# Kernel optimization log

Hardware: AMD Instinct MI355X
Metric: run time of the kernel (lower is better)

The kernel has to match this reference:

```python
import jax, jax.numpy as jnp
import numpy as np
from jax import lax

BN_EPS = 1e-3  # keras BatchNormalization default
DN = ('NHWC', 'HWIO', 'NHWC')


def setup_inputs() -> dict:
    key = jax.random.key(0)
    ks = jax.random.split(key, 8)
    B, H, W, C = 16, 224, 224, 96
    K = 3
    x = jax.random.normal(ks[0], (B, H, W, C), dtype=jnp.float32)
    dw_kernel = jax.random.normal(ks[1], (K, K, 1, C), dtype=jnp.float32) * 0.1
    dw_bias = jnp.zeros((C,), dtype=jnp.float32)
    pw_kernel = jax.random.normal(ks[2], (1, 1, C, C), dtype=jnp.float32) * 0.1
    pw_bias = jnp.zeros((C,), dtype=jnp.float32)
    gamma = jax.random.uniform(ks[3], (C,), dtype=jnp.float32, minval=0.5, maxval=1.5)
    beta = jax.random.normal(ks[4], (C,), dtype=jnp.float32) * 0.1
    moving_mean = jax.random.normal(ks[5], (C,), dtype=jnp.float32) * 0.1
    moving_var = jax.random.uniform(ks[6], (C,), dtype=jnp.float32, minval=0.5, maxval=1.5)
    return {
        'x': x, 'dw_kernel': dw_kernel, 'dw_bias': dw_bias,
        'pw_kernel': pw_kernel, 'pw_bias': pw_bias,
        'gamma': gamma, 'beta': beta,
        'moving_mean': moving_mean, 'moving_var': moving_var,
    }


def reference(x, dw_kernel, dw_bias, pw_kernel, pw_bias, gamma, beta, moving_mean, moving_var):
    C = x.shape[-1]
    stride = 1
    # ReLU at the start of the op
    y = jax.nn.relu(x)
    # Depthwise conv: feature_group_count = C, kernel HWIO = (K, K, 1, C)
    y = lax.conv_general_dilated(
        y, dw_kernel, window_strides=(stride, stride), padding='SAME',
        dimension_numbers=DN, feature_group_count=C)
    y = y + dw_bias
    # Pointwise 1x1 conv to C_curr channels
    y = lax.conv_general_dilated(
        y, pw_kernel, window_strides=(1, 1), padding='SAME',
        dimension_numbers=DN)
    y = y + pw_bias
    # BatchNormalization (inference mode: use moving statistics)
    inv = gamma * lax.rsqrt(moving_var + BN_EPS)
    y = y * inv + (beta - moving_mean * inv)
    return y
```

## Files before the change

kernel.cpp:

```cpp
#include <hip/hip_runtime.h>
#include <hip/hip_bf16.h>


#define BATCH 16
#define HH 224
#define WWD 224
#define CC 96
#define NPIX (BATCH*HH*WWD)
#define TILE 64
#define NBLK (NPIX/TILE)
#define NTHREADS 384
#define PAD 104

typedef __attribute__((ext_vector_type(8))) short short8;
typedef __attribute__((ext_vector_type(4))) float f32x4;

__device__ __forceinline__ unsigned short f2bf(float f){
    union{float f; unsigned u;} v; v.f = f;
    unsigned r = v.u + 0x7fffu + ((v.u >> 16) & 1u);
    return (unsigned short)(r >> 16);
}

__global__ __launch_bounds__(NTHREADS) void sepconv_kernel(
    const float* __restrict__ x,
    const float* __restrict__ dwk,
    const float* __restrict__ dwb,
    const float* __restrict__ pwk,
    const float* __restrict__ pwb,
    const float* __restrict__ gma,
    const float* __restrict__ bta,
    const float* __restrict__ mmean,
    const float* __restrict__ mvar,
    float* __restrict__ out)
{
    __shared__ __align__(16) unsigned short s_dw[TILE][PAD];
    __shared__ __align__(16) unsigned short s_pwT[CC][PAD];
    __shared__ float s_scale[CC];
    __shared__ float s_shift[CC];

    const int t  = threadIdx.x;
    const int p0 = blockIdx.x * TILE;

    for (int e = t; e < CC*CC; e += NTHREADS) {
        int ci = e / CC;
        int co = e - ci*CC;
        s_pwT[co][ci] = f2bf(pwk[e]);
    }
    if (t < CC) {
        float g  = gma[t];
        float be = bta[t];
        float mu = mmean[t];
        float va = mvar[t];
        float pb = pwb[t];
        float sc = g / sqrtf(va + 1e-3f);
        s_scale[t] = sc;
        s_shift[t] = (pb - mu) * sc + be;
    }

    #pragma unroll
    for (int it = 0; it < 2; ++it) {
        int i  = t + it*NTHREADS;
        int px = i / 12;
        int cg = i - px*12;
        int c0 = cg*8;
        int p  = p0 + px;
        int b  = p / (HH*WWD);
        int rem = p - b*(HH*WWD);
        int h  = rem / WWD;
        int w  = rem - h*WWD;

        float acc[8];
        {
            float4 b0 = *reinterpret_cast<const float4*>(dwb + c0);
            float4 b1 = *reinterpret_cast<const float4*>(dwb + c0 + 4);
            acc[0]=b0.x; acc[1]=b0.y; acc[2]=b0.z; acc[3]=b0.w;
            acc[4]=b1.x; acc[5]=b1.y; acc[6]=b1.z; acc[7]=b1.w;
        }
        #pragma unroll
        for (int kh = -1; kh <= 1; ++kh) {
            int h2 = h + kh;
            if ((unsigned)h2 >= HH) continue;
            #pragma unroll
            for (int kw = -1; kw <= 1; ++kw) {
                int w2 = w + kw;
                if ((unsigned)w2 >= WWD) continue;
                const float* xp = x + (size_t)((b*HH + h2)*WWD + w2)*CC + c0;
                const float* wp = dwk + ((kh+1)*3 + (kw+1))*CC + c0;
                float4 x0 = *reinterpret_cast<const float4*>(xp);
                float4 x1 = *reinterpret_cast<const float4*>(xp + 4);
                float4 w0 = *reinterpret_cast<const float4*>(wp);
                float4 w1 = *reinterpret_cast<const float4*>(wp + 4);
                acc[0] += fmaxf(x0.x, 0.f) * w0.x;
                acc[1] += fmaxf(x0.y, 0.f) * w0.y;
                acc[2] += fmaxf(x0.z, 0.f) * w0.z;
                acc[3] += fmaxf(x0.w, 0.f) * w0.w;
                acc[4] += fmaxf(x1.x, 0.f) * w1.x;
                acc[5] += fmaxf(x1.y, 0.f) * w1.y;
                acc[6] += fmaxf(x1.z, 0.f) * w1.z;
                acc[7] += fmaxf(x1.w, 0.f) * w1.w;
            }
        }
        uint4 sv;
        sv.x = (unsigned)f2bf(acc[0]) | ((unsigned)f2bf(acc[1]) << 16);
        sv.y = (unsigned)f2bf(acc[2]) | ((unsigned)f2bf(acc[3]) << 16);
        sv.z = (unsigned)f2bf(acc[4]) | ((unsigned)f2bf(acc[5]) << 16);
        sv.w = (unsigned)f2bf(acc[6]) | ((unsigned)f2bf(acc[7]) << 16);
        *reinterpret_cast<uint4*>(&s_dw[px][c0]) = sv;
    }

    __syncthreads();

    const int wave = t >> 6;
    const int lane = t & 63;
    const int col  = lane & 15;
    const int quad = lane >> 4;
    const int co   = wave*16 + col;

    short8 bfr[3];
    #pragma unroll
    for (int ks = 0; ks < 3; ++ks)
        bfr[ks] = *reinterpret_cast<const short8*>(&s_pwT[co][ks*32 + quad*8]);

    const float sc = s_scale[co];
    const float sh = s_shift[co];

    #pragma unroll
    for (int mt = 0; mt < 4; ++mt) {
        f32x4 acc = {0.f, 0.f, 0.f, 0.f};
        #pragma unroll
        for (int ks = 0; ks < 3; ++ks) {
            short8 afr = *reinterpret_cast<const short8*>(&s_dw[mt*16 + col][ks*32 + quad*8]);
            acc = __builtin_amdgcn_mfma_f32_16x16x32_bf16(afr, bfr[ks], acc, 0, 0, 0);
        }
        int prow = p0 + mt*16 + quad*4;
        #pragma unroll
        for (int r = 0; r < 4; ++r) {
            float v = acc[r]*sc + sh;
            out[(size_t)(prow + r)*CC + co] = v;
        }
    }
}

extern "C" void kernel_launch(void* const* d_in, const int* in_sizes, int n_in,
                              void* d_out, int out_size, void* d_ws, size_t ws_size,
                              hipStream_t stream)
{
    sepconv_kernel<<<NBLK, NTHREADS, 0, stream>>>(
        (const float*)d_in[0],
        (const float*)d_in[1],
        (const float*)d_in[2],
        (const float*)d_in[3],
        (const float*)d_in[4],
        (const float*)d_in[5],
        (const float*)d_in[6],
        (const float*)d_in[7],
        (const float*)d_in[8],
        (float*)d_out);
}
```

Measured before the change: 688.9 us.

## Use persistent XCD-banded waves computing depthwise conv directly into MFMA fragments

Replaces the one-block-per-64-pixel launch with a persistent grid of 1024 blocks. Each wave processes 16-pixel row tiles, and tiles are assigned in contiguous bands per XCD so neighbouring rows share L2. The depthwise result is computed straight into registers already in MFMA A-fragment layout, which removes the shared-memory staging buffer and its barrier. The pointwise weights are staged and converted once per block instead of once per 64 pixels. In exchange, each lane issues more scattered loads, register pressure is higher, and the band mapping assumes a particular XCD scheduling order.

Result: slower. 755.6 us (+9.7%).

```diff
diff --git a/kernel.cpp b/kernel.cpp
--- a/kernel.cpp
+++ b/kernel.cpp
@@ -6,10 +6,15 @@
 #define HH 224
 #define WWD 224
 #define CC 96
-#define NPIX (BATCH*HH*WWD)
-#define TILE 64
-#define NBLK (NPIX/TILE)
-#define NTHREADS 384
+#define ROWS (BATCH*HH)
+#define TPR 14
+#define NTILES (ROWS*TPR)
+#define NTHREADS 256
+#define WAVES 4
+#define NBLOCKS 1024
+#define NXCD 8
+#define TILES_PER_BAND (NTILES/NXCD)
+#define WAVES_PER_BAND ((NBLOCKS/NXCD)*WAVES)
 #define PAD 104
 
 typedef __attribute__((ext_vector_type(8))) short short8;
@@ -21,7 +26,28 @@
     return (unsigned short)(r >> 16);
 }
 
-__global__ __launch_bounds__(NTHREADS) void sepconv_kernel(
+__device__ __forceinline__ void tap_fma(const float* __restrict__ xp,
+                                        const float* wp,
+                                        float acc[3][8])
+{
+    #pragma unroll
+    for (int ks = 0; ks < 3; ++ks) {
+        float4 x0 = *reinterpret_cast<const float4*>(xp + ks*32);
+        float4 x1 = *reinterpret_cast<const float4*>(xp + ks*32 + 4);
+        float4 w0 = *reinterpret_cast<const float4*>(wp + ks*32);
+        float4 w1 = *reinterpret_cast<const float4*>(wp + ks*32 + 4);
+        acc[ks][0] += fmaxf(x0.x, 0.f) * w0.x;
+        acc[ks][1] += fmaxf(x0.y, 0.f) * w0.y;
+        acc[ks][2] += fmaxf(x0.z, 0.f) * w0.z;
+        acc[ks][3] += fmaxf(x0.w, 0.f) * w0.w;
+        acc[ks][4] += fmaxf(x1.x, 0.f) * w1.x;
+        acc[ks][5] += fmaxf(x1.y, 0.f) * w1.y;
+        acc[ks][6] += fmaxf(x1.z, 0.f) * w1.z;
+        acc[ks][7] += fmaxf(x1.w, 0.f) * w1.w;
+    }
+}
+
+__global__ __launch_bounds__(NTHREADS, 4) void sepconv_kernel(
     const float* __restrict__ x,
     const float* __restrict__ dwk,
     const float* __restrict__ dwb,
@@ -33,110 +59,97 @@
     const float* __restrict__ mvar,
     float* __restrict__ out)
 {
-    __shared__ __align__(16) unsigned short s_dw[TILE][PAD];
     __shared__ __align__(16) unsigned short s_pwT[CC][PAD];
-    __shared__ float s_scale[CC];
-    __shared__ float s_shift[CC];
+    __shared__ __align__(16) float s_dwk[9][CC];
+    __shared__ __align__(16) float s_dwb[CC];
+    __shared__ __align__(16) float s_scale[CC];
+    __shared__ __align__(16) float s_shift[CC];
 
-    const int t  = threadIdx.x;
-    const int p0 = blockIdx.x * TILE;
+    const int t = threadIdx.x;
 
     for (int e = t; e < CC*CC; e += NTHREADS) {
         int ci = e / CC;
         int co = e - ci*CC;
         s_pwT[co][ci] = f2bf(pwk[e]);
     }
+    for (int e = t; e < 9*CC; e += NTHREADS)
+        (&s_dwk[0][0])[e] = dwk[e];
     if (t < CC) {
-        float g  = gma[t];
-        float be = bta[t];
-        float mu = mmean[t];
-        float va = mvar[t];
-        float pb = pwb[t];
-        float sc = g / sqrtf(va + 1e-3f);
+        s_dwb[t] = dwb[t];
+        float sc = gma[t] / sqrtf(mvar[t] + 1e-3f);
         s_scale[t] = sc;
-        s_shift[t] = (pb - mu) * sc + be;
+        s_shift[t] = (pwb[t] - mmean[t]) * sc + bta[t];
     }
-
-    #pragma unroll
-    for (int it = 0; it < 2; ++it) {
-        int i  = t + it*NTHREADS;
-        int px = i / 12;
-        int cg = i - px*12;
-        int c0 = cg*8;
-        int p  = p0 + px;
-        int b  = p / (HH*WWD);
-        int rem = p - b*(HH*WWD);
-        int h  = rem / WWD;
-        int w  = rem - h*WWD;
-
-        float acc[8];
-        {
-            float4 b0 = *reinterpret_cast<const float4*>(dwb + c0);
-            float4 b1 = *reinterpret_cast<const float4*>(dwb + c0 + 4);
-            acc[0]=b0.x; acc[1]=b0.y; acc[2]=b0.z; acc[3]=b0.w;
-            acc[4]=b1.x; acc[5]=b1.y; acc[6]=b1.z; acc[7]=b1.w;
-        }
-        #pragma unroll
-        for (int kh = -1; kh <= 1; ++kh) {
-            int h2 = h + kh;
-            if ((unsigned)h2 >= HH) continue;
-            #pragma unroll
-            for (int kw = -1; kw <= 1; ++kw) {
-                int w2 = w + kw;
-                if ((unsigned)w2 >= WWD) continue;
-                const float* xp = x + (size_t)((b*HH + h2)*WWD + w2)*CC + c0;
-                const float* wp = dwk + ((kh+1)*3 + (kw+1))*CC + c0;
-                float4 x0 = *reinterpret_cast<const float4*>(xp);
-                float4 x1 = *reinterpret_cast<const float4*>(xp + 4);
-                float4 w0 = *reinterpret_cast<const float4*>(wp);
-                float4 w1 = *reinterpret_cast<const float4*>(wp + 4);
-                acc[0] += fmaxf(x0.x, 0.f) * w0.x;
-                acc[1] += fmaxf(x0.y, 0.f) * w0.y;
-                acc[2] += fmaxf(x0.z, 0.f) * w0.z;
-                acc[3] += fmaxf(x0.w, 0.f) * w0.w;
-                acc[4] += fmaxf(x1.x, 0.f) * w1.x;
-                acc[5] += fmaxf(x1.y, 0.f) * w1.y;
-                acc[6] += fmaxf(x1.z, 0.f) * w1.z;
-                acc[7] += fmaxf(x1.w, 0.f) * w1.w;
-            }
-        }
-        uint4 sv;
-        sv.x = (unsigned)f2bf(acc[0]) | ((unsigned)f2bf(acc[1]) << 16);
-        sv.y = (unsigned)f2bf(acc[2]) | ((unsigned)f2bf(acc[3]) << 16);
-        sv.z = (unsigned)f2bf(acc[4]) | ((unsigned)f2bf(acc[5]) << 16);
-        sv.w = (unsigned)f2bf(acc[6]) | ((unsigned)f2bf(acc[7]) << 16);
-        *reinterpret_cast<uint4*>(&s_dw[px][c0]) = sv;
-    }
-
     __syncthreads();
 
     const int wave = t >> 6;
     const int lane = t & 63;
     const int col  = lane & 15;
     const int quad = lane >> 4;
-    const int co   = wave*16 + col;
 
-    short8 bfr[3];
+    float scv[6], shv[6];
     #pragma unroll
-    for (int ks = 0; ks < 3; ++ks)
-        bfr[ks] = *reinterpret_cast<const short8*>(&s_pwT[co][ks*32 + quad*8]);
+    for (int nt = 0; nt < 6; ++nt) {
+        scv[nt] = s_scale[nt*16 + col];
+        shv[nt] = s_shift[nt*16 + col];
+    }
 
-    const float sc = s_scale[co];
-    const float sh = s_shift[co];
+    const int xcd = blockIdx.x & (NXCD-1);
+    const int lb  = blockIdx.x >> 3;
+    const int gw  = lb*WAVES + wave;
+    const int Tend = (xcd+1)*TILES_PER_BAND;
 
-    #pragma unroll
-    for (int mt = 0; mt < 4; ++mt) {
-        f32x4 acc = {0.f, 0.f, 0.f, 0.f};
+    for (int T = xcd*TILES_PER_BAND + gw; T < Tend; T += WAVES_PER_BAND) {
+        const int rrow = T / TPR;
+        const int wt   = T - rrow*TPR;
+        const int h    = rrow % HH;
+        const int w_me = wt*16 + col;
+        const float* xb = x + (size_t)(rrow*WWD + w_me)*CC + quad*8;
+
+        float acc[3][8];
         #pragma unroll
         for (int ks = 0; ks < 3; ++ks) {
-            short8 afr = *reinterpret_cast<const short8*>(&s_dw[mt*16 + col][ks*32 + quad*8]);
-            acc = __builtin_amdgcn_mfma_f32_16x16x32_bf16(afr, bfr[ks], acc, 0, 0, 0);
+            float4 b0 = *reinterpret_cast<const float4*>(&s_dwb[ks*32 + quad*8]);
+            float4 b1 = *reinterpret_cast<const float4*>(&s_dwb[ks*32 + quad*8 + 4]);
+            acc[ks][0]=b0.x; acc[ks][1]=b0.y; acc[ks][2]=b0.z; acc[ks][3]=b0.w;
+            acc[ks][4]=b1.x; acc[ks][5]=b1.y; acc[ks][6]=b1.z; acc[ks][7]=b1.w;
         }
-        int prow = p0 + mt*16 + quad*4;
+
         #pragma unroll
-        for (int r = 0; r < 4; ++r) {
-            float v = acc[r]*sc + sh;
-            out[(size_t)(prow + r)*CC + co] = v;
+        for (int kh = -1; kh <= 1; ++kh) {
+            const int h2 = h + kh;
+            if ((unsigned)h2 >= HH) continue;
+            const float* rp = xb + kh*(WWD*CC);
+            const float* wr = &s_dwk[(kh+1)*3][0] + quad*8;
+            if (w_me >= 1)       tap_fma(rp - CC, wr,        acc);
+                                 tap_fma(rp,      wr + CC,   acc);
+            if (w_me <= WWD-2)   tap_fma(rp + CC, wr + 2*CC, acc);
+        }
+
+        short8 afr[3];
+        #pragma unroll
+        for (int ks = 0; ks < 3; ++ks) {
+            union { short8 v; unsigned u[4]; } pk;
+            #pragma unroll
+            for (int j = 0; j < 4; ++j)
+                pk.u[j] = (unsigned)f2bf(acc[ks][2*j])
+                        | ((unsigned)f2bf(acc[ks][2*j+1]) << 16);
+            afr[ks] = pk.v;
+        }
+
+        float* ob = out + (size_t)(T*16 + quad*4)*CC + col;
+        #pragma unroll
+        for (int nt = 0; nt < 6; ++nt) {
+            f32x4 macc = {0.f, 0.f, 0.f, 0.f};
+            #pragma unroll
+            for (int ks = 0; ks < 3; ++ks) {
+                short8 bfr = *reinterpret_cast<const short8*>(
+                    &s_pwT[nt*16 + col][ks*32 + quad*8]);
+                macc = __builtin_amdgcn_mfma_f32_16x16x32_bf16(afr[ks], bfr, macc, 0, 0, 0);
+            }
+            #pragma unroll
+            for (int r2 = 0; r2 < 4; ++r2)
+                ob[r2*CC + nt*16] = macc[r2]*scv[nt] + shv[nt];
         }
     }
 }
@@ -145,7 +158,7 @@
                               void* d_out, int out_size, void* d_ws, size_t ws_size,
                               hipStream_t stream)
 {
-    sepconv_kernel<<<NBLK, NTHREADS, 0, stream>>>(
+    sepconv_kernel<<<NBLOCKS, NTHREADS, 0, stream>>>(
         (const float*)d_in[0],
         (const float*)d_in[1],
         (const float*)d_in[2],
```
